# Kernel optimization log

Measured on AMD Instinct MI355X. Metric: run time of the kernel, lower is better.

## Reference

```python
import jax, jax.numpy as jnp
import numpy as np
from jax import lax

KH, KW, PAD = 3, 3, 1  # kernel_size and paddings from init_kwargs


def _sign_pm1(v):
    # tf.sign with zeros mapped to -1
    return jnp.where(v > 0, jnp.float32(1.0), jnp.float32(-1.0)).astype(v.dtype)


def setup_inputs() -> dict:
    key = jax.random.key(0)
    k1, k2, k3 = jax.random.split(key, 3)
    x = jax.random.normal(k1, (32, 56, 56, 256), dtype=jnp.float32)
    kernel = jax.random.normal(k2, (KH, KW, 256, 256), dtype=jnp.float32) * 0.05
    bias = jax.random.normal(k3, (256,), dtype=jnp.float32) * 0.01
    return {"x": x, "kernel": kernel, "bias": bias}


def reference(x, kernel, bias):
    # pad input spatially (NHWC)
    xp = jnp.pad(x, ((0, 0), (PAD, PAD), (PAD, PAD), (0, 0)))

    # binarize kernel: static batch dim known -> alpha = mean(|W|) over (kh, kw, cin)
    bin_k = _sign_pm1(kernel)
    alpha = jnp.mean(jnp.abs(kernel), axis=(0, 1, 2))  # (Cout,)

    # binarize input: batch dim dynamic in TF -> beta = mean(|x|) over channels, keepdims
    bin_x = _sign_pm1(xp)                               # (N, H+2P, W+2P, C)
    beta = jnp.mean(jnp.abs(xp), axis=3, keepdims=True)  # (N, H+2P, W+2P, 1)

    # K = avg_pool(beta, kernel window, stride 1, VALID)
    K = lax.reduce_window(beta, jnp.float32(0.0), lax.add,
                          (1, KH, KW, 1), (1, 1, 1, 1), 'VALID') / (KH * KW)
    Ka = K * alpha  # (N, H, W, Cout) via broadcast

    conv = lax.conv_general_dilated(
        bin_x, bin_k, window_strides=(1, 1), padding='VALID',
        dimension_numbers=('NHWC', 'HWIO', 'NHWC'))  # (N, H, W, Cout)

    return conv * Ka + bias
```

## Files before the change

### kernel.cpp

```cpp
#include <hip/hip_runtime.h>
#include <cstdint>

#define N_ 32
#define H_ 56
#define W_ 56
#define C_ 256
#define HP 58
#define WP 58

__global__ __launch_bounds__(256) void pack_w(const float* __restrict__ k,
                                              uint64_t* __restrict__ kb,
                                              float* __restrict__ palpha) {
    int idx = blockIdx.x;
    int p = idx >> 2, j = idx & 3;
    int co = threadIdx.x;
    uint64_t bits = 0;
    float s = 0.f;
    #pragma unroll
    for (int b = 0; b < 64; ++b) {
        int ci = j * 64 + b;
        float v = k[(p * 256 + ci) * 256 + co];
        bits |= (uint64_t)(v > 0.f) << b;
        s += fabsf(v);
    }
    kb[idx * 256 + co] = bits;
    palpha[idx * 256 + co] = s;
}

__global__ void pack_x(const float* __restrict__ x, uint64_t* __restrict__ xb,
                       float* __restrict__ beta) {
    int bi = blockIdx.x;
    int n = bi / HP, y = bi % HP;
    int wave = threadIdx.x >> 6, lane = threadIdx.x & 63;
    for (int xc = wave; xc < WP; xc += 4) {
        bool inb = (y >= 1 && y <= H_ && xc >= 1 && xc <= W_);
        float v0 = 0.f, v1 = 0.f, v2 = 0.f, v3 = 0.f;
        if (inb) {
            const float* px = x + (((size_t)n * H_ + (y - 1)) * W_ + (xc - 1)) * C_;
            v0 = px[lane];
            v1 = px[64 + lane];
            v2 = px[128 + lane];
            v3 = px[192 + lane];
        }
        uint64_t m0 = __ballot(v0 > 0.f);
        uint64_t m1 = __ballot(v1 > 0.f);
        uint64_t m2 = __ballot(v2 > 0.f);
        uint64_t m3 = __ballot(v3 > 0.f);
        float s = fabsf(v0) + fabsf(v1) + fabsf(v2) + fabsf(v3);
        #pragma unroll
        for (int m = 32; m >= 1; m >>= 1) s += __shfl_xor(s, m, 64);
        size_t pix = (size_t)bi * WP + xc;
        if (lane < 4) {
            uint64_t mw = (lane == 0) ? m0 : (lane == 1) ? m1 : (lane == 2) ? m2 : m3;
            xb[pix * 4 + lane] = mw;
        }
        if (lane == 0) beta[pix] = s * (1.f / 256.f);
    }
}

__global__ __launch_bounds__(256, 4) void bconv(
        const uint64_t* __restrict__ xb, const float* __restrict__ beta,
        const uint64_t* __restrict__ kb, const float* __restrict__ palpha,
        const float* __restrict__ bias, float* __restrict__ out) {
    int bi = blockIdx.x;
    int n = bi / H_, h = bi % H_;
    int co = threadIdx.x;

    __shared__ __align__(16) uint64_t xs[3 * WP * 4];
    __shared__ float brow[3 * WP];
    __shared__ float bS[W_];

    const uint64_t* xsrc = xb + (size_t)(n * HP + h) * WP * 4;
    for (int i = threadIdx.x; i < 3 * WP * 4; i += 256) xs[i] = xsrc[i];
    const float* bsrc = beta + (size_t)(n * HP + h) * WP;
    for (int i = threadIdx.x; i < 3 * WP; i += 256) brow[i] = bsrc[i];
    __syncthreads();

    if (threadIdx.x < W_) {
        float s = 0.f;
        #pragma unroll
        for (int r = 0; r < 3; ++r)
            #pragma unroll
            for (int d = 0; d < 3; ++d) s += brow[r * WP + threadIdx.x + d];
        bS[threadIdx.x] = s * (1.f / 9.f);
    }

    float asum = 0.f;
    #pragma unroll
    for (int i = 0; i < 36; ++i) asum += palpha[i * 256 + co];
    float alpha = asum * (1.f / 2304.f);
    float bv = bias[co];
    __syncthreads();

    float* orow = out + (size_t)(n * H_ + h) * W_ * C_ + co;

    for (int chunk = 0; chunk < 4; ++chunk) {
        int w0 = chunk * 14;
        uint32_t acc[14];
        #pragma unroll
        for (int i = 0; i < 14; ++i) acc[i] = 0;

        for (int jp = 0; jp < 2; ++jp) {
            uint64_t kr0[9], kr1[9];
            #pragma unroll
            for (int t = 0; t < 9; ++t) {
                kr0[t] = kb[(t * 4 + 2 * jp) * 256 + co];
                kr1[t] = kb[(t * 4 + 2 * jp + 1) * 256 + co];
            }
            #pragma unroll
            for (int xi = 0; xi < 16; ++xi) {
                #pragma unroll
                for (int r = 0; r < 3; ++r) {
                    const uint64_t* px = &xs[(r * WP + w0 + xi) * 4 + 2 * jp];
                    uint64_t x0 = px[0], x1 = px[1];
                    #pragma unroll
                    for (int kw = 0; kw < 3; ++kw) {
                        int wl = xi - kw;
                        if (wl >= 0 && wl < 14) {
                            int t = r * 3 + kw;
                            acc[wl] += __popcll(x0 ^ kr0[t]) + __popcll(x1 ^ kr1[t]);
                        }
                    }
                }
            }
        }
        #pragma unroll
        for (int wl = 0; wl < 14; ++wl) {
            int w = w0 + wl;
            float conv = (float)(2304 - 2 * (int)acc[wl]);
            orow[(size_t)w * C_] = conv * bS[w] * alpha + bv;
        }
    }
}

extern "C" void kernel_launch(void* const* d_in, const int* in_sizes, int n_in,
                              void* d_out, int out_size, void* d_ws, size_t ws_size,
                              hipStream_t stream) {
    const float* x    = (const float*)d_in[0];
    const float* k    = (const float*)d_in[1];
    const float* bias = (const float*)d_in[2];
    float* out = (float*)d_out;

    char* ws = (char*)d_ws;
    uint64_t* kb     = (uint64_t*)(ws);
    float*    palpha = (float*)(ws + 73728);
    uint64_t* xb     = (uint64_t*)(ws + 110592);
    float*    beta   = (float*)(ws + 3555328);

    pack_w<<<36, 256, 0, stream>>>(k, kb, palpha);
    pack_x<<<N_ * HP, 256, 0, stream>>>(x, xb, beta);
    bconv<<<N_ * H_, 256, 0, stream>>>(xb, beta, kb, palpha, bias, out);
}
```

Measured before the change: 302.7 us.

## Split channel words across thread halves and vectorize input packing loads

```diff
diff --git a/kernel.cpp b/kernel.cpp
--- a/kernel.cpp
+++ b/kernel.cpp
@@ -7,6 +7,7 @@
 #define C_ 256
 #define HP 58
 #define WP 58
+
 
 __global__ __launch_bounds__(256) void pack_w(const float* __restrict__ k,
                                               uint64_t* __restrict__ kb,
@@ -18,35 +19,30 @@
     float s = 0.f;
     #pragma unroll
     for (int b = 0; b < 64; ++b) {
-        int ci = j * 64 + b;
-        float v = k[(p * 256 + ci) * 256 + co];
+        float v = k[(p * 256 + 4 * b + j) * 256 + co];
         bits |= (uint64_t)(v > 0.f) << b;
         s += fabsf(v);
     }
-    kb[idx * 256 + co] = bits;
+    kb[((size_t)p * 256 + co) * 4 + j] = bits;
     palpha[idx * 256 + co] = s;
 }
 
-__global__ void pack_x(const float* __restrict__ x, uint64_t* __restrict__ xb,
-                       float* __restrict__ beta) {
+__global__ __launch_bounds__(256) void pack_x(const float4* __restrict__ x4,
+                                              uint64_t* __restrict__ xb,
+                                              float* __restrict__ beta) {
     int bi = blockIdx.x;
     int n = bi / HP, y = bi % HP;
     int wave = threadIdx.x >> 6, lane = threadIdx.x & 63;
     for (int xc = wave; xc < WP; xc += 4) {
         bool inb = (y >= 1 && y <= H_ && xc >= 1 && xc <= W_);
-        float v0 = 0.f, v1 = 0.f, v2 = 0.f, v3 = 0.f;
-        if (inb) {
-            const float* px = x + (((size_t)n * H_ + (y - 1)) * W_ + (xc - 1)) * C_;
-            v0 = px[lane];
-            v1 = px[64 + lane];
-            v2 = px[128 + lane];
-            v3 = px[192 + lane];
-        }
-        uint64_t m0 = __ballot(v0 > 0.f);
-        uint64_t m1 = __ballot(v1 > 0.f);
-        uint64_t m2 = __ballot(v2 > 0.f);
-        uint64_t m3 = __ballot(v3 > 0.f);
-        float s = fabsf(v0) + fabsf(v1) + fabsf(v2) + fabsf(v3);
+        float4 v = make_float4(0.f, 0.f, 0.f, 0.f);
+        if (inb)
+            v = x4[(((size_t)n * H_ + (y - 1)) * W_ + (xc - 1)) * 64 + lane];
+        uint64_t m0 = __ballot(v.x > 0.f);
+        uint64_t m1 = __ballot(v.y > 0.f);
+        uint64_t m2 = __ballot(v.z > 0.f);
+        uint64_t m3 = __ballot(v.w > 0.f);
+        float s = fabsf(v.x) + fabsf(v.y) + fabsf(v.z) + fabsf(v.w);
         #pragma unroll
         for (int m = 32; m >= 1; m >>= 1) s += __shfl_xor(s, m, 64);
         size_t pix = (size_t)bi * WP + xc;
@@ -64,35 +60,44 @@
         const float* __restrict__ bias, float* __restrict__ out) {
     int bi = blockIdx.x;
     int n = bi / H_, h = bi % H_;
-    int co = threadIdx.x;
+    int tid = threadIdx.x;
+    int half = tid >> 7;
+    int col = tid & 127;
+    int co = (blockIdx.y << 7) | col;
 
     __shared__ __align__(16) uint64_t xs[3 * WP * 4];
     __shared__ float brow[3 * WP];
     __shared__ float bS[W_];
+    __shared__ uint32_t pb[128 * 15];
 
     const uint64_t* xsrc = xb + (size_t)(n * HP + h) * WP * 4;
-    for (int i = threadIdx.x; i < 3 * WP * 4; i += 256) xs[i] = xsrc[i];
+    for (int i = tid; i < 3 * WP * 2; i += 256)
+        ((ulonglong2*)xs)[i] = ((const ulonglong2*)xsrc)[i];
     const float* bsrc = beta + (size_t)(n * HP + h) * WP;
-    for (int i = threadIdx.x; i < 3 * WP; i += 256) brow[i] = bsrc[i];
+    for (int i = tid; i < 3 * WP; i += 256) brow[i] = bsrc[i];
     __syncthreads();
 
-    if (threadIdx.x < W_) {
+    if (tid < W_) {
         float s = 0.f;
         #pragma unroll
         for (int r = 0; r < 3; ++r)
             #pragma unroll
-            for (int d = 0; d < 3; ++d) s += brow[r * WP + threadIdx.x + d];
-        bS[threadIdx.x] = s * (1.f / 9.f);
+            for (int d = 0; d < 3; ++d) s += brow[r * WP + tid + d];
+        bS[tid] = s * (1.f / 9.f);
     }
 
+    uint64_t kr0[9], kr1[9];
+    #pragma unroll
+    for (int t = 0; t < 9; ++t) {
+        ulonglong2 kp = ((const ulonglong2*)kb)[((size_t)t * 256 + co) * 2 + half];
+        kr0[t] = kp.x;
+        kr1[t] = kp.y;
+    }
     float asum = 0.f;
     #pragma unroll
     for (int i = 0; i < 36; ++i) asum += palpha[i * 256 + co];
     float alpha = asum * (1.f / 2304.f);
     float bv = bias[co];
-    __syncthreads();
-
-    float* orow = out + (size_t)(n * H_ + h) * W_ * C_ + co;
 
     for (int chunk = 0; chunk < 4; ++chunk) {
         int w0 = chunk * 14;
@@ -100,35 +105,38 @@
         #pragma unroll
         for (int i = 0; i < 14; ++i) acc[i] = 0;
 
-        for (int jp = 0; jp < 2; ++jp) {
-            uint64_t kr0[9], kr1[9];
+        const uint64_t* base = &xs[w0 * 4 + 2 * half];
+        #pragma unroll
+        for (int xi = 0; xi < 16; ++xi) {
             #pragma unroll
-            for (int t = 0; t < 9; ++t) {
-                kr0[t] = kb[(t * 4 + 2 * jp) * 256 + co];
-                kr1[t] = kb[(t * 4 + 2 * jp + 1) * 256 + co];
-            }
-            #pragma unroll
-            for (int xi = 0; xi < 16; ++xi) {
+            for (int r = 0; r < 3; ++r) {
+                uint64_t x0 = base[(r * WP + xi) * 4];
+                uint64_t x1 = base[(r * WP + xi) * 4 + 1];
                 #pragma unroll
-                for (int r = 0; r < 3; ++r) {
-                    const uint64_t* px = &xs[(r * WP + w0 + xi) * 4 + 2 * jp];
-                    uint64_t x0 = px[0], x1 = px[1];
-                    #pragma unroll
-                    for (int kw = 0; kw < 3; ++kw) {
-                        int wl = xi - kw;
-                        if (wl >= 0 && wl < 14) {
-                            int t = r * 3 + kw;
-                            acc[wl] += __popcll(x0 ^ kr0[t]) + __popcll(x1 ^ kr1[t]);
-                        }
+                for (int kw = 0; kw < 3; ++kw) {
+                    int wl = xi - kw;
+                    if (wl >= 0 && wl < 14) {
+                        int t = r * 3 + kw;
+                        acc[wl] += __popcll(x0 ^ kr0[t]) + __popcll(x1 ^ kr1[t]);
                     }
                 }
             }
         }
-        #pragma unroll
-        for (int wl = 0; wl < 14; ++wl) {
-            int w = w0 + wl;
-            float conv = (float)(2304 - 2 * (int)acc[wl]);
-            orow[(size_t)w * C_] = conv * bS[w] * alpha + bv;
+
+        __syncthreads();
+        if (half == 1) {
+            #pragma unroll
+            for (int i = 0; i < 14; ++i) pb[col * 15 + i] = acc[i];
+        }
+        __syncthreads();
+        if (half == 0) {
+            #pragma unroll
+            for (int i = 0; i < 14; ++i) {
+                int w = w0 + i;
+                int tot = (int)(acc[i] + pb[col * 15 + i]);
+                float conv = (float)(2304 - 2 * tot);
+                out[((size_t)bi * W_ + w) * C_ + co] = conv * bS[w] * alpha + bv;
+            }
         }
     }
 }
@@ -148,6 +156,6 @@
     float*    beta   = (float*)(ws + 3555328);
 
     pack_w<<<36, 256, 0, stream>>>(k, kb, palpha);
-    pack_x<<<N_ * HP, 256, 0, stream>>>(x, xb, beta);
-    bconv<<<N_ * H_, 256, 0, stream>>>(xb, beta, kb, palpha, bias, out);
+    pack_x<<<N_ * HP, 256, 0, stream>>>((const float4*)x, xb, beta);
+    bconv<<<dim3(N_ * H_, 2), 256, 0, stream>>>(xb, beta, kb, palpha, bias, out);
 }
```

Result: faster. 296.6 us (-2.0%).
